# Optimization experiments

Hardware: AMD Instinct MI355X
Metric: run time of the kernel (lower is better)

Reference implementation:

```python
import jax, jax.numpy as jnp
import numpy as np

jax.config.update('jax_enable_x64', True)  # original uses complex128

N_Q = 8          # qubits -> Hilbert dim 256
N_L = 6          # circuit layers
DIM = 2 ** N_Q
BATCH = 16384


def _kron_b(a, b):
    # batched kron: a (..., m, m), b (..., n, n) -> (..., m*n, m*n)
    m, n = a.shape[-1], b.shape[-1]
    out = jnp.einsum('...ij,...ab->...iajb', a, b)
    return out.reshape(a.shape[:-2] + (m * n, m * n))


def _hadamard_full():
    h = jnp.array([[1.0, 1.0], [1.0, -1.0]], jnp.complex128) / 2 ** 0.5
    H = jnp.array([[1.0]], jnp.complex128)
    for _ in range(N_Q):
        H = jnp.kron(H, h)
    return H


def _cnots():
    I2 = jnp.eye(2, dtype=jnp.complex128)
    Z = jnp.array([[1.0, 0.0], [0.0, -1.0]], jnp.complex128)
    X = jnp.array([[0.0, 1.0], [1.0, 0.0]], jnp.complex128)
    mats = []
    for n in range(N_Q - 1):
        m = n + 1
        s = jnp.eye(2 ** n, dtype=jnp.complex128)
        s = jnp.kron(s, I2 - Z)
        s = jnp.kron(s, jnp.eye(2 ** (m - n - 1), dtype=jnp.complex128))
        s = jnp.kron(s, I2 - X)
        s = jnp.kron(s, jnp.eye(2 ** (N_Q - m - 1), dtype=jnp.complex128))
        # NOTE: /2**0.2 (not sqrt(2)) reproduced exactly from the source
        mats.append((jnp.eye(DIM, dtype=jnp.complex128) + 1j * s) / 2 ** 0.2)
    return mats


def _get_U(q_x, q_z, cnots, H):
    q_x = q_x.astype(jnp.float64)
    q_z = q_z.astype(jnp.float64)
    cx, sx = jnp.cos(q_x / 2.0), jnp.sin(q_x / 2.0)
    cz, sz = jnp.cos(q_z / 2.0), jnp.sin(q_z / 2.0)
    zero = jnp.zeros(cx.shape, jnp.complex128)
    # per source: r?(t) = cos(t/2) I + 1j sin(t/2) Pauli (note the +1j in rz)
    rz = jnp.stack([jnp.stack([cz + 1j * sz, zero], -1),
                    jnp.stack([zero, cz - 1j * sz], -1)], -2)  # (N_l, N_q, 2, 2)
    rx = jnp.stack([jnp.stack([cx + 0j, 1j * sx], -1),
                    jnp.stack([1j * sx, cx + 0j], -1)], -2)
    M = jnp.einsum('lqab,lqbc->lqac', rz, rx)  # rz @ rx per (layer, qubit)
    r = M[:, 0]
    for j in range(1, N_Q):  # kron chain over qubits, qubit 0 leftmost
        r = _kron_b(r, M[:, j])  # (N_l, DIM, DIM)
    U = jnp.eye(DIM, dtype=jnp.complex128)
    for l in range(N_L):
        d = jnp.eye(DIM, dtype=jnp.complex128)
        for n in range(N_Q - 1):
            d = d @ cnots[n]
            d = d @ r[l]
        U = U @ d
    return U @ H


def _f(q_x, q_z, c_embed, idx, cnots, H):
    # NOTE: c_embed is shadowed (never actually used) in the original source; kept for fidelity.
    U = _get_U(q_x, q_z, cnots, H)
    # Original: out += c[i] * sum_n A[n,n] * s[b,n]^2 with A = U^H Z_i U and s one-hot.
    # diag(U^H Z_i U)[n] = sum_m z_i[m] |U[m,n]|^2  (same math, no full matmul needed)
    absU2 = U.real ** 2 + U.imag ** 2  # (DIM, DIM) float64
    m = jnp.arange(DIM)
    bits = (m[None, :] >> (N_Q - 1 - jnp.arange(N_Q)[:, None])) & 1  # (N_q, DIM)
    zdiag = (1.0 - 2.0 * bits).astype(jnp.float64)
    D = zdiag @ absU2  # (N_q, DIM): D[i, n] = diag(U^H Z_i U)[n]
    # the source shadows `c` with the kron (one-hot) state of the LAST batch sample;
    # c[i] for i < N_q is 1 iff that sample's basis index equals i, else 0
    c_shadow = (jnp.arange(DIM)[:N_Q] == idx[-1]).astype(jnp.complex128)
    return jnp.einsum('i,ib->b', c_shadow, D[:, idx].astype(jnp.complex128))


def setup_inputs():
    key = jax.random.key(0)
    ks = jax.random.split(key, 7)
    x = jax.random.normal(ks[0], (BATCH, N_Q), jnp.float32)
    # make the last sample's basis index = 2^N_q - 1 (>= N_q) deterministically so the
    # shadowed-c path is the stable (all-zero) branch, avoiding exp overflow from the
    # non-unitary /2**0.2 cnot normalization in the source
    x = x.at[-1].set(jnp.abs(x[-1]) + 1.0)
    return {
        'x': x,
        'q_x1': jax.random.normal(ks[1], (N_L, N_Q), jnp.float32),
        'q_z1': jax.random.normal(ks[2], (N_L, N_Q), jnp.float32),
        'q_x2': jax.random.normal(ks[3], (N_L, N_Q), jnp.float32),
        'q_z2': jax.random.normal(ks[4], (N_L, N_Q), jnp.float32),
        'c1': jax.random.normal(ks[5], (1, N_Q), jnp.float32),
        'c2': jax.random.normal(ks[6], (1, N_Q), jnp.float32),
    }


def reference(x, q_x1, q_z1, q_x2, q_z2, c1, c2):
    cnots = _cnots()
    H = _hadamard_full()
    bits = (x > 0).astype(jnp.int32)  # (B, N_q)
    w = (2 ** (N_Q - 1 - jnp.arange(N_Q))).astype(jnp.int32)
    idx = bits @ w  # basis index of each sample's kron of one-hot vectors
    f1 = _f(q_x1, q_z1, c1, idx, cnots, H)
    f2 = _f(q_x2, q_z2, c2, idx, cnots, H)
    return jnp.exp(f1 + 1j * f2)
```

## Files before the change

### kernel.cpp

```cpp
#include <hip/hip_runtime.h>
#include <math.h>


#define NQ 8
#define NL 6
#define QDIM 256
#define BATCH 16384

#define OFF_U 0
#define OFF_T 131072
#define OFF_R 262144
#define OFF_V 393216

__device__ __forceinline__ int compute_idx(const float* __restrict__ xrow) {
  int v = 0;
#pragma unroll
  for (int j = 0; j < NQ; ++j)
    v |= (xrow[j] > 0.0f) ? (1 << (NQ - 1 - j)) : 0;
  return v;
}

__global__ __launch_bounds__(256) void heavy_kernel(
    const float* __restrict__ x,
    const float* __restrict__ qx1, const float* __restrict__ qz1,
    const float* __restrict__ qx2, const float* __restrict__ qz2,
    double* __restrict__ W)
{
  const int idxl = compute_idx(x + (size_t)(BATCH - 1) * NQ);
  if (idxl >= NQ) return;

  const int t = threadIdx.x;
  double* U = W + OFF_U;
  double* T = W + OFF_T;
  double* R = W + OFF_R;
  const double ainv = 0.8705505632961241;

  for (int circ = 0; circ < 2; ++circ) {
    const float* qx = circ ? qx2 : qx1;
    const float* qz = circ ? qz2 : qz1;

    for (int c = 0; c < QDIM; ++c) {
      U[((size_t)t * QDIM + c) * 2 + 0] = (c == t) ? 1.0 : 0.0;
      U[((size_t)t * QDIM + c) * 2 + 1] = 0.0;
    }

    for (int l = 0; l < NL; ++l) {
      double Mr[NQ][2][2], Mi[NQ][2][2];
      for (int j = 0; j < NQ; ++j) {
        double hx = 0.5 * (double)qx[l * NQ + j];
        double hz = 0.5 * (double)qz[l * NQ + j];
        double cx = cos(hx), sx = sin(hx), cz = cos(hz), sz = sin(hz);
        Mr[j][0][0] =  cx * cz;  Mi[j][0][0] =  cx * sz;
        Mr[j][0][1] = -sx * sz;  Mi[j][0][1] =  sx * cz;
        Mr[j][1][0] =  sx * sz;  Mi[j][1][0] =  sx * cz;
        Mr[j][1][1] =  cx * cz;  Mi[j][1][1] = -cx * sz;
      }

      __syncthreads();
      for (int c = 0; c < QDIM; ++c) {
        double ar = 1.0, ai = 0.0;
        for (int j = 0; j < NQ; ++j) {
          int rb = (t >> (NQ - 1 - j)) & 1;
          int cb = (c >> (NQ - 1 - j)) & 1;
          double br = Mr[j][rb][cb], bi = Mi[j][rb][cb];
          double nr = ar * br - ai * bi;
          ai = ar * bi + ai * br;
          ar = nr;
        }
        R[((size_t)t * QDIM + c) * 2 + 0] = ar;
        R[((size_t)t * QDIM + c) * 2 + 1] = ai;
      }
      __syncthreads();

      for (int n = 0; n < NQ - 1; ++n) {
        const int bn = NQ - 1 - n;
        const int fm = 1 << (NQ - 2 - n);
        for (int c = 0; c < QDIM; ++c) {
          size_t pc = ((size_t)t * QDIM + c) * 2;
          if (((c >> bn) & 1) == 0) {
            U[pc + 0] *= ainv;
            U[pc + 1] *= ainv;
          } else if ((c & fm) == 0) {
            int c2 = c | fm;
            size_t p2 = ((size_t)t * QDIM + c2) * 2;
            double ar = U[pc + 0], ai = U[pc + 1];
            double br = U[p2 + 0], bi = U[p2 + 1];
            U[pc + 0] = (ar - 2.0 * ai + 2.0 * bi) * ainv;
            U[pc + 1] = (ai + 2.0 * ar - 2.0 * br) * ainv;
            U[p2 + 0] = (br - 2.0 * bi + 2.0 * ai) * ainv;
            U[p2 + 1] = (bi + 2.0 * br - 2.0 * ar) * ainv;
          }
        }
        for (int c = 0; c < QDIM; ++c) {
          double ar = 0.0, ai = 0.0;
          for (int k = 0; k < QDIM; ++k) {
            double ur = U[((size_t)t * QDIM + k) * 2 + 0];
            double ui = U[((size_t)t * QDIM + k) * 2 + 1];
            double rr = R[((size_t)k * QDIM + c) * 2 + 0];
            double ri = R[((size_t)k * QDIM + c) * 2 + 1];
            ar += ur * rr - ui * ri;
            ai += ur * ri + ui * rr;
          }
          T[((size_t)t * QDIM + c) * 2 + 0] = ar;
          T[((size_t)t * QDIM + c) * 2 + 1] = ai;
        }
        for (int c = 0; c < QDIM; ++c) {
          U[((size_t)t * QDIM + c) * 2 + 0] = T[((size_t)t * QDIM + c) * 2 + 0];
          U[((size_t)t * QDIM + c) * 2 + 1] = T[((size_t)t * QDIM + c) * 2 + 1];
        }
      }
    }

    for (int c = 0; c < QDIM; ++c) {
      double ar = 0.0, ai = 0.0;
      for (int k = 0; k < QDIM; ++k) {
        double s = (__popc(k & c) & 1) ? -1.0 : 1.0;
        ar += U[((size_t)t * QDIM + k) * 2 + 0] * s;
        ai += U[((size_t)t * QDIM + k) * 2 + 1] * s;
      }
      T[((size_t)t * QDIM + c) * 2 + 0] = ar * 0.0625;
      T[((size_t)t * QDIM + c) * 2 + 1] = ai * 0.0625;
    }
    __syncthreads();

    {
      double acc = 0.0;
      for (int m = 0; m < QDIM; ++m) {
        double s = ((m >> (NQ - 1 - idxl)) & 1) ? -1.0 : 1.0;
        double re = T[((size_t)m * QDIM + t) * 2 + 0];
        double im = T[((size_t)m * QDIM + t) * 2 + 1];
        acc += s * (re * re + im * im);
      }
      W[OFF_V + circ * QDIM + t] = acc;
    }
    __syncthreads();
  }
}

__global__ __launch_bounds__(256) void out_kernel(
    const float* __restrict__ x, const double* __restrict__ W,
    float* __restrict__ out, int n_complex, int interleaved)
{
  int b = blockIdx.x * blockDim.x + threadIdx.x;
  if (b >= n_complex) return;

  const int idxl = compute_idx(x + (size_t)(BATCH - 1) * NQ);

  float re = 1.0f, im = 0.0f;
  if (idxl < NQ) {
    const int ib = compute_idx(x + (size_t)b * NQ);
    double f1 = W[OFF_V + 0 * QDIM + ib];
    double f2 = W[OFF_V + 1 * QDIM + ib];
    double e = exp(f1);
    re = (float)(e * cos(f2));
    im = (float)(e * sin(f2));
  }

  if (interleaved) {
    float2 v; v.x = re; v.y = im;
    reinterpret_cast<float2*>(out)[b] = v;
  } else {
    out[b] = re;
  }
}

extern "C" void kernel_launch(void* const* d_in, const int* in_sizes, int n_in,
                              void* d_out, int out_size, void* d_ws, size_t ws_size,
                              hipStream_t stream) {
  const float* x   = (const float*)d_in[0];
  const float* qx1 = (const float*)d_in[1];
  const float* qz1 = (const float*)d_in[2];
  const float* qx2 = (const float*)d_in[3];
  const float* qz2 = (const float*)d_in[4];

  double* W  = (double*)d_ws;
  float* out = (float*)d_out;

  heavy_kernel<<<1, 256, 0, stream>>>(x, qx1, qz1, qx2, qz2, W);

  const int interleaved = (out_size == 2 * BATCH) ? 1 : 0;
  const int n = interleaved ? (out_size / 2) : out_size;
  const int blocks = (n + 255) / 256;
  out_kernel<<<blocks, 256, 0, stream>>>(x, W, out, n, interleaved);
}
```

Measured before the change: 65.27 us.

## Fuse heavy and output kernels into one launch with per-block workspace slices

Merges the single-block circuit kernel and the output kernel into one launch of up to 16 blocks. Each block redundantly computes the circuit in its own workspace slice when the general path is taken, then writes its share of outputs. In the stable branch (last index >= 8) it writes constant (1,0) pairs with float4 stores. This removes a kernel launch and the inter-kernel dependency, at the cost of redundant heavy work per block in the general case.

```diff
diff --git a/kernel.cpp b/kernel.cpp
--- a/kernel.cpp
+++ b/kernel.cpp
@@ -11,6 +11,7 @@
 #define OFF_T 131072
 #define OFF_R 262144
 #define OFF_V 393216
+#define SLICE_DOUBLES 393728
 
 __device__ __forceinline__ int compute_idx(const float* __restrict__ xrow) {
   int v = 0;
@@ -20,16 +21,12 @@
   return v;
 }
 
-__global__ __launch_bounds__(256) void heavy_kernel(
-    const float* __restrict__ x,
+__device__ void heavy_path(
+    int t, int idxl,
     const float* __restrict__ qx1, const float* __restrict__ qz1,
     const float* __restrict__ qx2, const float* __restrict__ qz2,
     double* __restrict__ W)
 {
-  const int idxl = compute_idx(x + (size_t)(BATCH - 1) * NQ);
-  if (idxl >= NQ) return;
-
-  const int t = threadIdx.x;
   double* U = W + OFF_U;
   double* T = W + OFF_T;
   double* R = W + OFF_R;
@@ -135,32 +132,53 @@
     }
     __syncthreads();
   }
-}
-
-__global__ __launch_bounds__(256) void out_kernel(
-    const float* __restrict__ x, const double* __restrict__ W,
-    float* __restrict__ out, int n_complex, int interleaved)
+  __syncthreads();
+}
+
+__global__ __launch_bounds__(256) void fused_kernel(
+    const float* __restrict__ x,
+    const float* __restrict__ qx1, const float* __restrict__ qz1,
+    const float* __restrict__ qx2, const float* __restrict__ qz2,
+    double* __restrict__ Wbase,
+    float* __restrict__ out, int n_complex, int interleaved, int per_thread)
 {
-  int b = blockIdx.x * blockDim.x + threadIdx.x;
-  if (b >= n_complex) return;
-
+  const int t = threadIdx.x;
   const int idxl = compute_idx(x + (size_t)(BATCH - 1) * NQ);
 
-  float re = 1.0f, im = 0.0f;
-  if (idxl < NQ) {
-    const int ib = compute_idx(x + (size_t)b * NQ);
-    double f1 = W[OFF_V + 0 * QDIM + ib];
-    double f2 = W[OFF_V + 1 * QDIM + ib];
-    double e = exp(f1);
-    re = (float)(e * cos(f2));
-    im = (float)(e * sin(f2));
+  double* W = Wbase + (size_t)blockIdx.x * SLICE_DOUBLES;
+  const bool general = (idxl < NQ);
+  if (general)
+    heavy_path(t, idxl, qx1, qz1, qx2, qz2, W);
+
+  const int base = (blockIdx.x * blockDim.x + t) * per_thread;
+
+  if (!general && interleaved && per_thread == 4 && base + 4 <= n_complex &&
+      (((uintptr_t)out) & 15) == 0) {
+    float4 v; v.x = 1.0f; v.y = 0.0f; v.z = 1.0f; v.w = 0.0f;
+    float4* o4 = reinterpret_cast<float4*>(out) + base / 2;
+    o4[0] = v;
+    o4[1] = v;
+    return;
   }
 
-  if (interleaved) {
-    float2 v; v.x = re; v.y = im;
-    reinterpret_cast<float2*>(out)[b] = v;
-  } else {
-    out[b] = re;
+  for (int r = 0; r < per_thread; ++r) {
+    int b = base + r;
+    if (b >= n_complex) break;
+    float re = 1.0f, im = 0.0f;
+    if (general) {
+      const int ib = compute_idx(x + (size_t)b * NQ);
+      double f1 = W[OFF_V + 0 * QDIM + ib];
+      double f2 = W[OFF_V + 1 * QDIM + ib];
+      double e = exp(f1);
+      re = (float)(e * cos(f2));
+      im = (float)(e * sin(f2));
+    }
+    if (interleaved) {
+      float2 v; v.x = re; v.y = im;
+      reinterpret_cast<float2*>(out)[b] = v;
+    } else {
+      out[b] = re;
+    }
   }
 }
 
@@ -176,10 +194,15 @@
   double* W  = (double*)d_ws;
   float* out = (float*)d_out;
 
-  heavy_kernel<<<1, 256, 0, stream>>>(x, qx1, qz1, qx2, qz2, W);
-
   const int interleaved = (out_size == 2 * BATCH) ? 1 : 0;
   const int n = interleaved ? (out_size / 2) : out_size;
-  const int blocks = (n + 255) / 256;
-  out_kernel<<<blocks, 256, 0, stream>>>(x, W, out, n, interleaved);
-}
+
+  const size_t slice_bytes = (size_t)SLICE_DOUBLES * sizeof(double);
+  int max_blocks = (int)(ws_size / slice_bytes);
+  if (max_blocks < 1) max_blocks = 1;
+  int nblocks = 16 < max_blocks ? 16 : max_blocks;
+  int per_thread = (n + nblocks * 256 - 1) / (nblocks * 256);
+
+  fused_kernel<<<nblocks, 256, 0, stream>>>(x, qx1, qz1, qx2, qz2, W, out,
+                                            n, interleaved, per_thread);
+}
```

New measurement: 64.86 us. No clear change (-0.6%).
